# Performance work log

Hardware: AMD Instinct MI355X
Metric: run time of the kernel (lower is better)

The kernel has to match this reference:

```python
import jax, jax.numpy as jnp
import numpy as np

D = 512
H = 8
HD = D // H

def setup_inputs() -> dict:
    key = jax.random.key(0)
    ks = jax.random.split(key, 16)
    B, L = 8, 384
    s = 1.0 / np.sqrt(D)
    inp = {
        "hidden_states": jax.random.normal(ks[0], (B, L, D), jnp.float32),
        "position_embeddings": jax.random.normal(ks[1], (L, L, D), jnp.float32),
        "attention_mask": jnp.ones((B, L), jnp.int32),
        "ln_g": jnp.ones((D,), jnp.float32),
        "ln_b": jnp.zeros((D,), jnp.float32),
        "Wq": jax.random.normal(ks[2], (D, D), jnp.float32) * s,
        "bq": jnp.zeros((D,), jnp.float32),
        "Wk": jax.random.normal(ks[3], (D, D), jnp.float32) * s,
        "bk": jnp.zeros((D,), jnp.float32),
        "Wv": jax.random.normal(ks[4], (D, D), jnp.float32) * s,
        "bv": jnp.zeros((D,), jnp.float32),
        "Wpos": jax.random.normal(ks[5], (D, D), jnp.float32) * s,
        "pos_bias_u": jax.random.normal(ks[6], (H, HD), jnp.float32) * 0.02,
        "pos_bias_v": jax.random.normal(ks[7], (H, HD), jnp.float32) * 0.02,
        "Wo": jax.random.normal(ks[8], (D, D), jnp.float32) * s,
        "bo": jnp.zeros((D,), jnp.float32),
    }
    return inp

def _layernorm(x, g, b, eps=1e-5):
    mu = jnp.mean(x, axis=-1, keepdims=True)
    var = jnp.var(x, axis=-1, keepdims=True)
    return (x - mu) * jax.lax.rsqrt(var + eps) * g + b

def reference(hidden_states, position_embeddings, attention_mask,
              ln_g, ln_b, Wq, bq, Wk, bk, Wv, bv, Wpos,
              pos_bias_u, pos_bias_v, Wo, bo):
    B, L, _ = hidden_states.shape
    x = _layernorm(hidden_states, ln_g, ln_b)
    # projections -> (B, L, H, HD)
    q = (x @ Wq.T + bq).reshape(B, L, H, HD)
    k = (x @ Wk.T + bk).reshape(B, L, H, HD)
    v = (x @ Wv.T + bv).reshape(B, L, H, HD)
    # relative position projection -> (H, L, L, HD); pos[h, i, j, d]
    pos = (position_embeddings @ Wpos.T).reshape(L, L, H, HD)
    pos = jnp.transpose(pos, (2, 0, 1, 3))
    q_u = q + pos_bias_u  # (B, L, H, HD)
    q_v = q + pos_bias_v
    # content score: ac[b,h,i,j] = sum_d q_u[b,i,h,d] * k[b,j,h,d]
    scores_ac = jnp.einsum('bihd,bjhd->bhij', q_u, k)
    # positional score (torch broadcast semantics): bd[b,h,i,j] = sum_d q_v[b,j,h,d] * pos[h,i,j,d]
    scores_bd = jnp.einsum('bjhd,hijd->bhij', q_v, pos)
    scores = (scores_ac + scores_bd) / np.sqrt(HD)
    mask = attention_mask[:, None, None, :]  # (B,1,1,L)
    scores = jnp.where(mask == 0, jnp.finfo(scores.dtype).min, scores)
    probs = jax.nn.softmax(scores, axis=-1)
    ctx = jnp.einsum('bhij,bjhd->bihd', probs, v).reshape(B, L, D)
    return ctx @ Wo.T + bo
```

## Files before the change

kernel.cpp:

```cpp
#include <hip/hip_runtime.h>
#include <hip/hip_bf16.h>

#define DEV __device__ __forceinline__

typedef short short8 __attribute__((ext_vector_type(8)));
typedef float f32x4 __attribute__((ext_vector_type(4)));
typedef unsigned short ushort4v __attribute__((ext_vector_type(4)));
typedef unsigned short u16;

DEV u16 f2b(float x){ __hip_bfloat16 h = __float2bfloat16(x); u16 u; __builtin_memcpy(&u, &h, 2); return u; }

DEV int swz(int row, int cb){ return row*128 + (cb ^ ((row & 7) << 4)); }
DEV int swz768(int row, int byte_in_row){ return row*768 + (byte_in_row ^ ((row & 7) << 4)); }

DEV short8 ldfrag(const u16* s, int row, int kbf){
  return *(const short8*)((const char*)s + swz(row, kbf*2));
}
DEV void st16(u16* s, int row, int cb, short8 v){
  *(short8*)((char*)s + swz(row, cb)) = v;
}
DEV f32x4 MFMA(short8 a, short8 b, f32x4 c){
  return __builtin_amdgcn_mfma_f32_16x16x32_bf16(a, b, c, 0, 0, 0);
}

template<int R>
DEV void stage_bf16(u16* lds, const u16* g, size_t rstride, int tid){
  #pragma unroll
  for (int c = tid; c < R*8; c += 256){
    int row = c >> 3, k = c & 7;
    short8 v = *(const short8*)(g + (size_t)row*rstride + k*8);
    st16(lds, row, k*16, v);
  }
}

template<int R>
DEV void stage_f32(u16* lds, const float* g, size_t rstride, int tid){
  #pragma unroll
  for (int c = tid; c < R*8; c += 256){
    int row = c >> 3, k = c & 7;
    const float* p = g + (size_t)row*rstride + k*8;
    f32x4 f0 = *(const f32x4*)p;
    f32x4 f1 = *(const f32x4*)(p + 4);
    short8 v;
    #pragma unroll
    for (int t = 0; t < 4; ++t){ v[t] = (short)f2b(f0[t]); v[t+4] = (short)f2b(f1[t]); }
    st16(lds, row, k*16, v);
  }
}

template<int MI, int NI>
DEV void mma_step(const u16* As, int ar0, const u16* Bs, int br0, f32x4 (&acc)[MI][NI], int lane){
  int r = lane & 15, kb = (lane >> 4) * 8;
  #pragma unroll
  for (int kk = 0; kk < 64; kk += 32){
    short8 a[MI], b[NI];
    #pragma unroll
    for (int mi = 0; mi < MI; ++mi) a[mi] = ldfrag(As, ar0 + mi*16 + r, kk + kb);
    #pragma unroll
    for (int ni = 0; ni < NI; ++ni) b[ni] = ldfrag(Bs, br0 + ni*16 + r, kk + kb);
    #pragma unroll
    for (int mi = 0; mi < MI; ++mi)
      #pragma unroll
      for (int ni = 0; ni < NI; ++ni)
        acc[mi][ni] = MFMA(a[mi], b[ni], acc[mi][ni]);
  }
}

__global__ __launch_bounds__(256) void k_ln(const float* __restrict__ hs, const float* __restrict__ g,
                                            const float* __restrict__ bb, u16* __restrict__ xbf){
  int lane = threadIdx.x & 63, wid = threadIdx.x >> 6;
  int row = blockIdx.x * 4 + wid;
  const float* p = hs + (size_t)row * 512;
  f32x4 v0 = ((const f32x4*)p)[lane];
  f32x4 v1 = ((const f32x4*)p)[lane + 64];
  float s = 0.f, s2 = 0.f;
  #pragma unroll
  for (int t = 0; t < 4; ++t){ s += v0[t] + v1[t]; s2 += v0[t]*v0[t] + v1[t]*v1[t]; }
  #pragma unroll
  for (int off = 32; off; off >>= 1){ s += __shfl_xor(s, off); s2 += __shfl_xor(s2, off); }
  float mu = s * (1.0f/512.0f);
  float var = s2 * (1.0f/512.0f) - mu*mu;
  float rs = rsqrtf(var + 1e-5f);
  int e0 = lane * 4, e1 = 256 + e0;
  ushort4v o0, o1;
  #pragma unroll
  for (int t = 0; t < 4; ++t){
    o0[t] = f2b((v0[t]-mu)*rs*g[e0+t]+bb[e0+t]);
    o1[t] = f2b((v1[t]-mu)*rs*g[e1+t]+bb[e1+t]);
  }
  *(ushort4v*)(xbf + (size_t)row*512 + e0) = o0;
  *(ushort4v*)(xbf + (size_t)row*512 + e1) = o1;
}

__global__ __launch_bounds__(256) void k_wpt(const float* __restrict__ Wpos, u16* __restrict__ Wpt){
  int idx = blockIdx.x * 256 + threadIdx.x;
  int o = idx >> 9, e = idx & 511;
  int h = o >> 6, d = o & 63;
  Wpt[((size_t)h*512 + e)*64 + d] = f2b(Wpos[idx]);
}

__global__ __launch_bounds__(256) void k_qkv(const u16* __restrict__ xbf,
    const float* __restrict__ Wq, const float* __restrict__ Wk, const float* __restrict__ Wv,
    const float* __restrict__ bq, const float* __restrict__ bk, const float* __restrict__ bv,
    const float* __restrict__ pbu, const float* __restrict__ pbv,
    u16* __restrict__ qu, u16* __restrict__ qv, u16* __restrict__ kkb, u16* __restrict__ vt){
  __shared__ __align__(16) u16 As[128*64];
  __shared__ __align__(16) u16 Bs[128*64];
  int tid = threadIdx.x, lane = tid & 63, wid = tid >> 6;
  int t0 = blockIdx.x * 128, n0 = blockIdx.y * 128, z = blockIdx.z;
  const float* W    = (z==0) ? Wq : (z==1) ? Wk : Wv;
  const float* bias = (z==0) ? bq : (z==1) ? bk : bv;
  f32x4 acc[4][4] = {};
  for (int k0 = 0; k0 < 512; k0 += 64){
    stage_bf16<128>(As, xbf + (size_t)t0*512 + k0, 512, tid);
    stage_f32<128>(Bs, W + (size_t)n0*512 + k0, 512, tid);
    __syncthreads();
    mma_step<4,4>(As, (wid>>1)*64, Bs, (wid&1)*64, acc, lane);
    __syncthreads();
  }
  int r = lane & 15, half = lane >> 4;
  #pragma unroll
  for (int mi = 0; mi < 4; ++mi)
  #pragma unroll
  for (int ni = 0; ni < 4; ++ni){
    int n = n0 + (wid&1)*64 + ni*16 + r;
    int h = n >> 6, d = n & 63;
    int m0 = t0 + (wid>>1)*64 + mi*16 + half*4;
    #pragma unroll
    for (int q = 0; q < 4; ++q){
      int t = m0 + q, b = t / 384, i = t - b*384;
      float v = acc[mi][ni][q] + bias[n];
      if (z == 0){
        qu[((size_t)(b*8+h)*384 + i)*64 + d] = f2b(v + pbu[n]);
        qv[((size_t)h*3072 + t)*64 + d]      = f2b(v + pbv[n]);
      } else if (z == 1){
        kkb[((size_t)(b*8+h)*384 + i)*64 + d] = f2b(v);
      } else {
        vt[((size_t)(b*8+h)*64 + d)*384 + i] = f2b(v);
      }
    }
  }
}

__global__ __launch_bounds__(256) void k_qw(const u16* __restrict__ qv, const u16* __restrict__ Wpt,
                                            u16* __restrict__ qW){
  __shared__ __align__(16) u16 As[128*64];
  __shared__ __align__(16) u16 Bs[128*64];
  int tid = threadIdx.x, lane = tid & 63, wid = tid >> 6;
  int t0 = blockIdx.x * 128, e0 = blockIdx.y * 128, h = blockIdx.z;
  f32x4 acc[4][4] = {};
  stage_bf16<128>(As, qv + ((size_t)h*3072 + t0)*64, 64, tid);
  stage_bf16<128>(Bs, Wpt + ((size_t)h*512 + e0)*64, 64, tid);
  __syncthreads();
  mma_step<4,4>(As, (wid>>1)*64, Bs, (wid&1)*64, acc, lane);
  int r = lane & 15, half = lane >> 4;
  #pragma unroll
  for (int mi = 0; mi < 4; ++mi)
  #pragma unroll
  for (int ni = 0; ni < 4; ++ni){
    int e = e0 + (wid&1)*64 + ni*16 + r;
    int m0 = t0 + (wid>>1)*64 + mi*16 + half*4;
    #pragma unroll
    for (int q = 0; q < 4; ++q){
      int t = m0 + q, b = t / 384, j = t - b*384;
      int bh = b*8 + h;
      qW[((size_t)bh*384 + j)*512 + e] = f2b(acc[mi][ni][q]);
    }
  }
}

__global__ __launch_bounds__(256, 3) void k_bd(const u16* __restrict__ qW, const float* __restrict__ P,
                                               float* __restrict__ Sbd){
  __shared__ __align__(16) u16 As[64*256];
  int tid = threadIdx.x, lane = tid & 63, wid = tid >> 6;
  int r = lane & 15, half = lane >> 4;
  int ib = blockIdx.x * 192, j = blockIdx.y;

  const float* Bp[3];
  #pragma unroll
  for (int ni = 0; ni < 3; ++ni){
    int i = ib + wid*48 + ni*16 + r;
    Bp[ni] = P + ((size_t)i*384 + j)*512 + half*8;
  }
  const u16* Ag = qW + (size_t)j*512;

  f32x4 acc[4][3] = {};
  #pragma unroll
  for (int kh = 0; kh < 2; ++kh){
    if (kh) __syncthreads();
    #pragma unroll
    for (int s = 0; s < 8; ++s){
      int c = tid + s*256;
      int bh = c >> 5, c16 = c & 31;
      short8 v = *(const short8*)(Ag + (size_t)bh*(384*512) + kh*256 + c16*8);
      *(short8*)((char*)As + bh*512 + ((c16*16) ^ ((bh & 7) << 4))) = v;
    }
    __syncthreads();
    #pragma unroll
    for (int k32 = 0; k32 < 8; ++k32){
      int e0 = kh*256 + k32*32;
      short8 bfr[3];
      #pragma unroll
      for (int ni = 0; ni < 3; ++ni){
        f32x4 f0 = *(const f32x4*)(Bp[ni] + e0);
        f32x4 f1 = *(const f32x4*)(Bp[ni] + e0 + 4);
        #pragma unroll
        for (int t = 0; t < 4; ++t){ bfr[ni][t] = (short)f2b(f0[t]); bfr[ni][t+4] = (short)f2b(f1[t]); }
      }
      #pragma unroll
      for (int mi = 0; mi < 4; ++mi){
        int row = mi*16 + r;
        short8 afr = *(const short8*)((const char*)As + row*512 + ((k32*64 + half*16) ^ ((row & 7) << 4)));
        #pragma unroll
        for (int ni = 0; ni < 3; ++ni)
          acc[mi][ni] = MFMA(afr, bfr[ni], acc[mi][ni]);
      }
    }
  }
  #pragma unroll
  for (int mi = 0; mi < 4; ++mi)
  #pragma unroll
  for (int ni = 0; ni < 3; ++ni){
    int i = ib + wid*48 + ni*16 + r;
    #pragma unroll
    for (int q = 0; q < 4; ++q){
      int bh = mi*16 + half*4 + q;
      Sbd[((size_t)j*64 + bh)*384 + i] = acc[mi][ni][q];
    }
  }
}

__global__ __launch_bounds__(256) void k_fin(const u16* __restrict__ qu, const u16* __restrict__ kkb,
                                             const u16* __restrict__ vt, const float* __restrict__ Sbd,
                                             const int* __restrict__ mask, u16* __restrict__ ctx){
  __shared__ __align__(16) char lds[72*1024];
  __shared__ float smbuf[2][4][2][16];
  u16* Ks = (u16*)lds;
  u16* Qs = (u16*)(lds + 48*1024);
  u16* Ps = (u16*)lds;
  u16* Vs = (u16*)(lds + 24*1024);
  int tid = threadIdx.x, lane = tid & 63, wid = tid >> 6;
  int r = lane & 15, half = lane >> 4;
  int i0 = blockIdx.x * 32, bh = blockIdx.y, b = bh >> 3, h = bh & 7;

  stage_bf16<384>(Ks, kkb + (size_t)bh*384*64, 64, tid);
  stage_bf16<32>(Qs, qu + ((size_t)bh*384 + i0)*64, 64, tid);
  __syncthreads();

  f32x4 acc[6][2] = {};
  mma_step<6,2>(Ks, wid*96, Qs, 0, acc, lane);

  int jw = wid*96 + half*4;
  #pragma unroll
  for (int mi = 0; mi < 6; ++mi){
    #pragma unroll
    for (int q = 0; q < 4; ++q){
      int j = jw + mi*16 + q;
      bool dead = (mask[b*384 + j] == 0);
      const float* srow = Sbd + ((size_t)j*64 + bh)*384 + i0;
      #pragma unroll
      for (int ni = 0; ni < 2; ++ni){
        float v = (acc[mi][ni][q] + srow[ni*16 + r]) * 0.125f;
        acc[mi][ni][q] = dead ? -3.402823466e38f : v;
      }
    }
  }

  short8 vreg[12];
  #pragma unroll
  for (int c = 0; c < 12; ++c){
    int cc = tid + c*256;
    int d = cc / 48, jc = cc - d*48;
    vreg[c] = *(const short8*)(vt + ((size_t)bh*64 + d)*384 + jc*8);
  }

  float mx[2];
  #pragma unroll
  for (int ni = 0; ni < 2; ++ni){
    float m = -3.402823466e38f;
    #pragma unroll
    for (int mi = 0; mi < 6; ++mi){
      f32x4 a = acc[mi][ni];
      m = fmaxf(m, fmaxf(fmaxf(a[0],a[1]), fmaxf(a[2],a[3])));
    }
    m = fmaxf(m, __shfl_xor(m, 16));
    m = fmaxf(m, __shfl_xor(m, 32));
    mx[ni] = m;
  }
  if (lane < 16){ smbuf[0][wid][0][r] = mx[0]; smbuf[0][wid][1][r] = mx[1]; }
  __syncthreads();
  #pragma unroll
  for (int ni = 0; ni < 2; ++ni)
    mx[ni] = fmaxf(fmaxf(smbuf[0][0][ni][r], smbuf[0][1][ni][r]),
                   fmaxf(smbuf[0][2][ni][r], smbuf[0][3][ni][r]));

  float sum[2] = {0.f, 0.f};
  #pragma unroll
  for (int ni = 0; ni < 2; ++ni){
    #pragma unroll
    for (int mi = 0; mi < 6; ++mi)
      #pragma unroll
      for (int q = 0; q < 4; ++q){
        float e = __expf(acc[mi][ni][q] - mx[ni]);
        acc[mi][ni][q] = e; sum[ni] += e;
      }
    sum[ni] += __shfl_xor(sum[ni], 16);
    sum[ni] += __shfl_xor(sum[ni], 32);
  }
  if (lane < 16){ smbuf[1][wid][0][r] = sum[0]; smbuf[1][wid][1][r] = sum[1]; }
  __syncthreads();
  float inv[2];
  #pragma unroll
  for (int ni = 0; ni < 2; ++ni)
    inv[ni] = 1.0f / (smbuf[1][0][ni][r] + smbuf[1][1][ni][r] + smbuf[1][2][ni][r] + smbuf[1][3][ni][r]);

  #pragma unroll
  for (int mi = 0; mi < 6; ++mi){
    int jb = jw + mi*16;
    #pragma unroll
    for (int ni = 0; ni < 2; ++ni){
      int i = ni*16 + r;
      ushort4v pk;
      #pragma unroll
      for (int q = 0; q < 4; ++q) pk[q] = f2b(acc[mi][ni][q] * inv[ni]);
      *(ushort4v*)((char*)Ps + swz768(i, jb*2)) = pk;
    }
  }
  #pragma unroll
  for (int c = 0; c < 12; ++c){
    int cc = tid + c*256;
    int d = cc / 48, jc = cc - d*48;
    *(short8*)((char*)Vs + swz768(d, jc*16)) = vreg[c];
  }
  __syncthreads();

  f32x4 acc2[2] = {};
  #pragma unroll
  for (int ks = 0; ks < 384; ks += 32){
    int j0 = ks + half*8;
    short8 bfr = *(const short8*)((const char*)Vs + swz768(wid*16 + r, j0*2));
    #pragma unroll
    for (int mi = 0; mi < 2; ++mi){
      short8 afr = *(const short8*)((const char*)Ps + swz768(mi*16 + r, j0*2));
      acc2[mi] = MFMA(afr, bfr, acc2[mi]);
    }
  }
  #pragma unroll
  for (int mi = 0; mi < 2; ++mi)
    #pragma unroll
    for (int q = 0; q < 4; ++q){
      int i = i0 + mi*16 + half*4 + q;
      int d = wid*16 + r;
      ctx[((size_t)(b*384 + i))*512 + h*64 + d] = f2b(acc2[mi][q]);
    }
}

__global__ __launch_bounds__(256) void k_out(const u16* __restrict__ ctx, const float* __restrict__ Wo,
                                             const float* __restrict__ bo, float* __restrict__ out){
  __shared__ __align__(16) u16 As[128*64];
  __shared__ __align__(16) u16 Bs[128*64];
  int tid = threadIdx.x, lane = tid & 63, wid = tid >> 6;
  int t0 = blockIdx.x * 128, n0 = blockIdx.y * 128;
  f32x4 acc[4][4] = {};
  for (int k0 = 0; k0 < 512; k0 += 64){
    stage_bf16<128>(As, ctx + (size_t)t0*512 + k0, 512, tid);
    stage_f32<128>(Bs, Wo + (size_t)n0*512 + k0, 512, tid);
    __syncthreads();
    mma_step<4,4>(As, (wid>>1)*64, Bs, (wid&1)*64, acc, lane);
    __syncthreads();
  }
  int r = lane & 15, half = lane >> 4;
  #pragma unroll
  for (int mi = 0; mi < 4; ++mi)
  #pragma unroll
  for (int ni = 0; ni < 4; ++ni){
    int n = n0 + (wid&1)*64 + ni*16 + r;
    int m0 = t0 + (wid>>1)*64 + mi*16 + half*4;
    #pragma unroll
    for (int q = 0; q < 4; ++q){
      int t = m0 + q;
      out[(size_t)t*512 + n] = acc[mi][ni][q] + bo[n];
    }
  }
}

extern "C" void kernel_launch(void* const* d_in, const int* in_sizes, int n_in,
                              void* d_out, int out_size, void* d_ws, size_t ws_size,
                              hipStream_t stream) {
  const float* hs   = (const float*)d_in[0];
  const float* P    = (const float*)d_in[1];
  const int*   mask = (const int*)d_in[2];
  const float* ln_g = (const float*)d_in[3];
  const float* ln_b = (const float*)d_in[4];
  const float* Wq   = (const float*)d_in[5];
  const float* bq   = (const float*)d_in[6];
  const float* Wk   = (const float*)d_in[7];
  const float* bk   = (const float*)d_in[8];
  const float* Wv   = (const float*)d_in[9];
  const float* bv   = (const float*)d_in[10];
  const float* Wpos = (const float*)d_in[11];
  const float* pbu  = (const float*)d_in[12];
  const float* pbv  = (const float*)d_in[13];
  const float* Wo   = (const float*)d_in[14];
  const float* bo   = (const float*)d_in[15];
  float* out = (float*)d_out;

  char* w = (char*)d_ws;
  u16* xbf = (u16*)w;   w += (size_t)3072*512*2;
  u16* qu  = (u16*)w;   w += (size_t)3072*512*2;
  u16* qv  = (u16*)w;   w += (size_t)3072*512*2;
  u16* kkb = (u16*)w;   w += (size_t)3072*512*2;
  u16* vt  = (u16*)w;   w += (size_t)3072*512*2;
  u16* Wpt = (u16*)w;   w += (size_t)8*512*64*2;
  u16* ctx = (u16*)w;   w += (size_t)3072*512*2;
  u16* qW  = (u16*)w;   w += (size_t)64*384*512*2;
  float* Sbd = (float*)w; w += (size_t)64*384*384*4;

  k_ln <<<768, 256, 0, stream>>>(hs, ln_g, ln_b, xbf);
  k_wpt<<<1024, 256, 0, stream>>>(Wpos, Wpt);
  k_qkv<<<dim3(24,4,3), 256, 0, stream>>>(xbf, Wq, Wk, Wv, bq, bk, bv, pbu, pbv, qu, qv, kkb, vt);
  k_qw <<<dim3(24,4,8), 256, 0, stream>>>(qv, Wpt, qW);
  k_bd <<<dim3(2,384), 256, 0, stream>>>(qW, P, Sbd);
  k_fin<<<dim3(12,64), 256, 0, stream>>>(qu, kkb, vt, Sbd, mask, ctx);
  k_out<<<dim3(24,4), 256, 0, stream>>>(ctx, Wo, bo, out);
}
```

Measured before the change: 196.0 us.

## Fuse layernorm and Wpos transpose into GEMMs, batch k_fin rows, retile k_out

LayerNorm is folded into the QKV GEMM: each block computes row statistics and normalizes hidden states while staging the A tile. The Wpos bf16 transpose is done inside k_qw's staging, which removes two kernel launches and the xbf/Wpt intermediate buffers. k_fin now handles 96 query rows per block in three sub-tiles, so K and V are staged once and reused across them. k_out moves to 64x64 tiles to launch more blocks. The costs are redundant LayerNorm statistics across the 12 blocks per row tile, uncoalesced strided Wpos reads, and more LDS per k_fin block, which lowers occupancy.

```diff
diff --git a/kernel.cpp b/kernel.cpp
--- a/kernel.cpp
+++ b/kernel.cpp
@@ -66,57 +66,65 @@
   }
 }
 
-__global__ __launch_bounds__(256) void k_ln(const float* __restrict__ hs, const float* __restrict__ g,
-                                            const float* __restrict__ bb, u16* __restrict__ xbf){
-  int lane = threadIdx.x & 63, wid = threadIdx.x >> 6;
-  int row = blockIdx.x * 4 + wid;
-  const float* p = hs + (size_t)row * 512;
-  f32x4 v0 = ((const f32x4*)p)[lane];
-  f32x4 v1 = ((const f32x4*)p)[lane + 64];
-  float s = 0.f, s2 = 0.f;
-  #pragma unroll
-  for (int t = 0; t < 4; ++t){ s += v0[t] + v1[t]; s2 += v0[t]*v0[t] + v1[t]*v1[t]; }
-  #pragma unroll
-  for (int off = 32; off; off >>= 1){ s += __shfl_xor(s, off); s2 += __shfl_xor(s2, off); }
-  float mu = s * (1.0f/512.0f);
-  float var = s2 * (1.0f/512.0f) - mu*mu;
-  float rs = rsqrtf(var + 1e-5f);
-  int e0 = lane * 4, e1 = 256 + e0;
-  ushort4v o0, o1;
-  #pragma unroll
-  for (int t = 0; t < 4; ++t){
-    o0[t] = f2b((v0[t]-mu)*rs*g[e0+t]+bb[e0+t]);
-    o1[t] = f2b((v1[t]-mu)*rs*g[e1+t]+bb[e1+t]);
-  }
-  *(ushort4v*)(xbf + (size_t)row*512 + e0) = o0;
-  *(ushort4v*)(xbf + (size_t)row*512 + e1) = o1;
-}
-
-__global__ __launch_bounds__(256) void k_wpt(const float* __restrict__ Wpos, u16* __restrict__ Wpt){
-  int idx = blockIdx.x * 256 + threadIdx.x;
-  int o = idx >> 9, e = idx & 511;
-  int h = o >> 6, d = o & 63;
-  Wpt[((size_t)h*512 + e)*64 + d] = f2b(Wpos[idx]);
-}
-
-__global__ __launch_bounds__(256) void k_qkv(const u16* __restrict__ xbf,
+__global__ __launch_bounds__(256) void k_qkv(const float* __restrict__ hs,
+    const float* __restrict__ lg, const float* __restrict__ lb,
     const float* __restrict__ Wq, const float* __restrict__ Wk, const float* __restrict__ Wv,
     const float* __restrict__ bq, const float* __restrict__ bk, const float* __restrict__ bv,
     const float* __restrict__ pbu, const float* __restrict__ pbv,
     u16* __restrict__ qu, u16* __restrict__ qv, u16* __restrict__ kkb, u16* __restrict__ vt){
   __shared__ __align__(16) u16 As[128*64];
   __shared__ __align__(16) u16 Bs[128*64];
+  __shared__ float ps[2][128], ps2[2][128], mus[128], rss[128];
+  __shared__ float gs[512], bss[512];
   int tid = threadIdx.x, lane = tid & 63, wid = tid >> 6;
   int t0 = blockIdx.x * 128, n0 = blockIdx.y * 128, z = blockIdx.z;
   const float* W    = (z==0) ? Wq : (z==1) ? Wk : Wv;
   const float* bias = (z==0) ? bq : (z==1) ? bk : bv;
+
+  {
+    int row = tid & 127, hf = tid >> 7;
+    const f32x4* p = (const f32x4*)(hs + (size_t)(t0+row)*512 + hf*256);
+    float s = 0.f, s2 = 0.f;
+    #pragma unroll 8
+    for (int c = 0; c < 64; ++c){
+      f32x4 v = p[c];
+      #pragma unroll
+      for (int t = 0; t < 4; ++t){ s += v[t]; s2 += v[t]*v[t]; }
+    }
+    ps[hf][row] = s; ps2[hf][row] = s2;
+  }
+  gs[tid] = lg[tid]; gs[tid+256] = lg[tid+256];
+  bss[tid] = lb[tid]; bss[tid+256] = lb[tid+256];
+  __syncthreads();
+  if (tid < 128){
+    float S = ps[0][tid] + ps[1][tid], S2 = ps2[0][tid] + ps2[1][tid];
+    float mu = S * (1.0f/512.0f);
+    float var = S2 * (1.0f/512.0f) - mu*mu;
+    mus[tid] = mu; rss[tid] = rsqrtf(var + 1e-5f);
+  }
+
   f32x4 acc[4][4] = {};
   for (int k0 = 0; k0 < 512; k0 += 64){
-    stage_bf16<128>(As, xbf + (size_t)t0*512 + k0, 512, tid);
+    __syncthreads();
+    #pragma unroll
+    for (int c = tid; c < 1024; c += 256){
+      int rw = c >> 3, k = c & 7;
+      const float* pp = hs + (size_t)(t0+rw)*512 + k0 + k*8;
+      f32x4 f0 = *(const f32x4*)pp;
+      f32x4 f1 = *(const f32x4*)(pp + 4);
+      float mu = mus[rw], rs = rss[rw];
+      short8 v;
+      #pragma unroll
+      for (int t = 0; t < 4; ++t){
+        int e = k0 + k*8 + t;
+        v[t]   = (short)f2b((f0[t]-mu)*rs*gs[e]   + bss[e]);
+        v[t+4] = (short)f2b((f1[t]-mu)*rs*gs[e+4] + bss[e+4]);
+      }
+      st16(As, rw, k*16, v);
+    }
     stage_f32<128>(Bs, W + (size_t)n0*512 + k0, 512, tid);
     __syncthreads();
     mma_step<4,4>(As, (wid>>1)*64, Bs, (wid&1)*64, acc, lane);
-    __syncthreads();
   }
   int r = lane & 15, half = lane >> 4;
   #pragma unroll
@@ -142,7 +150,7 @@
   }
 }
 
-__global__ __launch_bounds__(256) void k_qw(const u16* __restrict__ qv, const u16* __restrict__ Wpt,
+__global__ __launch_bounds__(256) void k_qw(const u16* __restrict__ qv, const float* __restrict__ Wpos,
                                             u16* __restrict__ qW){
   __shared__ __align__(16) u16 As[128*64];
   __shared__ __align__(16) u16 Bs[128*64];
@@ -150,7 +158,15 @@
   int t0 = blockIdx.x * 128, e0 = blockIdx.y * 128, h = blockIdx.z;
   f32x4 acc[4][4] = {};
   stage_bf16<128>(As, qv + ((size_t)h*3072 + t0)*64, 64, tid);
-  stage_bf16<128>(Bs, Wpt + ((size_t)h*512 + e0)*64, 64, tid);
+  #pragma unroll
+  for (int c = tid; c < 1024; c += 256){
+    int e = c >> 3, k = c & 7;
+    short8 v;
+    #pragma unroll
+    for (int t = 0; t < 8; ++t)
+      v[t] = (short)f2b(Wpos[(size_t)(h*64 + k*8 + t)*512 + e0 + e]);
+    st16(Bs, e, k*16, v);
+  }
   __syncthreads();
   mma_step<4,4>(As, (wid>>1)*64, Bs, (wid&1)*64, acc, lane);
   int r = lane & 15, half = lane >> 4;
@@ -233,149 +249,143 @@
 __global__ __launch_bounds__(256) void k_fin(const u16* __restrict__ qu, const u16* __restrict__ kkb,
                                              const u16* __restrict__ vt, const float* __restrict__ Sbd,
                                              const int* __restrict__ mask, u16* __restrict__ ctx){
-  __shared__ __align__(16) char lds[72*1024];
+  __shared__ __align__(16) u16 Ks[384*64];
+  __shared__ __align__(16) u16 Qs[96*64];
+  __shared__ __align__(16) u16 Vs[64*384];
+  __shared__ __align__(16) u16 Ps[32*384];
   __shared__ float smbuf[2][4][2][16];
-  u16* Ks = (u16*)lds;
-  u16* Qs = (u16*)(lds + 48*1024);
-  u16* Ps = (u16*)lds;
-  u16* Vs = (u16*)(lds + 24*1024);
   int tid = threadIdx.x, lane = tid & 63, wid = tid >> 6;
   int r = lane & 15, half = lane >> 4;
-  int i0 = blockIdx.x * 32, bh = blockIdx.y, b = bh >> 3, h = bh & 7;
+  int i0 = blockIdx.x * 96, bh = blockIdx.y, b = bh >> 3, h = bh & 7;
 
   stage_bf16<384>(Ks, kkb + (size_t)bh*384*64, 64, tid);
-  stage_bf16<32>(Qs, qu + ((size_t)bh*384 + i0)*64, 64, tid);
+  stage_bf16<96>(Qs, qu + ((size_t)bh*384 + i0)*64, 64, tid);
+  #pragma unroll
+  for (int c = tid; c < 3072; c += 256){
+    int d = c / 48, jc = c - d*48;
+    short8 v = *(const short8*)(vt + ((size_t)bh*64 + d)*384 + jc*8);
+    *(short8*)((char*)Vs + swz768(d, jc*16)) = v;
+  }
   __syncthreads();
 
-  f32x4 acc[6][2] = {};
-  mma_step<6,2>(Ks, wid*96, Qs, 0, acc, lane);
-
-  int jw = wid*96 + half*4;
-  #pragma unroll
-  for (int mi = 0; mi < 6; ++mi){
-    #pragma unroll
-    for (int q = 0; q < 4; ++q){
-      int j = jw + mi*16 + q;
-      bool dead = (mask[b*384 + j] == 0);
-      const float* srow = Sbd + ((size_t)j*64 + bh)*384 + i0;
+  for (int sub = 0; sub < 3; ++sub){
+    int i0s = i0 + sub*32;
+    f32x4 acc[6][2] = {};
+    mma_step<6,2>(Ks, wid*96, Qs, sub*32, acc, lane);
+
+    int jw = wid*96 + half*4;
+    #pragma unroll
+    for (int mi = 0; mi < 6; ++mi){
+      #pragma unroll
+      for (int q = 0; q < 4; ++q){
+        int j = jw + mi*16 + q;
+        bool dead = (mask[b*384 + j] == 0);
+        const float* srow = Sbd + ((size_t)j*64 + bh)*384 + i0s;
+        #pragma unroll
+        for (int ni = 0; ni < 2; ++ni){
+          float v = (acc[mi][ni][q] + srow[ni*16 + r]) * 0.125f;
+          acc[mi][ni][q] = dead ? -3.402823466e38f : v;
+        }
+      }
+    }
+
+    float mx[2];
+    #pragma unroll
+    for (int ni = 0; ni < 2; ++ni){
+      float m = -3.402823466e38f;
+      #pragma unroll
+      for (int mi = 0; mi < 6; ++mi){
+        f32x4 a = acc[mi][ni];
+        m = fmaxf(m, fmaxf(fmaxf(a[0],a[1]), fmaxf(a[2],a[3])));
+      }
+      m = fmaxf(m, __shfl_xor(m, 16));
+      m = fmaxf(m, __shfl_xor(m, 32));
+      mx[ni] = m;
+    }
+    if (lane < 16){ smbuf[0][wid][0][r] = mx[0]; smbuf[0][wid][1][r] = mx[1]; }
+    __syncthreads();
+    #pragma unroll
+    for (int ni = 0; ni < 2; ++ni)
+      mx[ni] = fmaxf(fmaxf(smbuf[0][0][ni][r], smbuf[0][1][ni][r]),
+                     fmaxf(smbuf[0][2][ni][r], smbuf[0][3][ni][r]));
+
+    float sum[2] = {0.f, 0.f};
+    #pragma unroll
+    for (int ni = 0; ni < 2; ++ni){
+      #pragma unroll
+      for (int mi = 0; mi < 6; ++mi)
+        #pragma unroll
+        for (int q = 0; q < 4; ++q){
+          float e = __expf(acc[mi][ni][q] - mx[ni]);
+          acc[mi][ni][q] = e; sum[ni] += e;
+        }
+      sum[ni] += __shfl_xor(sum[ni], 16);
+      sum[ni] += __shfl_xor(sum[ni], 32);
+    }
+    if (lane < 16){ smbuf[1][wid][0][r] = sum[0]; smbuf[1][wid][1][r] = sum[1]; }
+    __syncthreads();
+    float inv[2];
+    #pragma unroll
+    for (int ni = 0; ni < 2; ++ni)
+      inv[ni] = 1.0f / (smbuf[1][0][ni][r] + smbuf[1][1][ni][r] + smbuf[1][2][ni][r] + smbuf[1][3][ni][r]);
+
+    #pragma unroll
+    for (int mi = 0; mi < 6; ++mi){
+      int jb = jw + mi*16;
       #pragma unroll
       for (int ni = 0; ni < 2; ++ni){
-        float v = (acc[mi][ni][q] + srow[ni*16 + r]) * 0.125f;
-        acc[mi][ni][q] = dead ? -3.402823466e38f : v;
-      }
-    }
-  }
-
-  short8 vreg[12];
-  #pragma unroll
-  for (int c = 0; c < 12; ++c){
-    int cc = tid + c*256;
-    int d = cc / 48, jc = cc - d*48;
-    vreg[c] = *(const short8*)(vt + ((size_t)bh*64 + d)*384 + jc*8);
-  }
-
-  float mx[2];
-  #pragma unroll
-  for (int ni = 0; ni < 2; ++ni){
-    float m = -3.402823466e38f;
-    #pragma unroll
-    for (int mi = 0; mi < 6; ++mi){
-      f32x4 a = acc[mi][ni];
-      m = fmaxf(m, fmaxf(fmaxf(a[0],a[1]), fmaxf(a[2],a[3])));
-    }
-    m = fmaxf(m, __shfl_xor(m, 16));
-    m = fmaxf(m, __shfl_xor(m, 32));
-    mx[ni] = m;
-  }
-  if (lane < 16){ smbuf[0][wid][0][r] = mx[0]; smbuf[0][wid][1][r] = mx[1]; }
-  __syncthreads();
-  #pragma unroll
-  for (int ni = 0; ni < 2; ++ni)
-    mx[ni] = fmaxf(fmaxf(smbuf[0][0][ni][r], smbuf[0][1][ni][r]),
-                   fmaxf(smbuf[0][2][ni][r], smbuf[0][3][ni][r]));
-
-  float sum[2] = {0.f, 0.f};
-  #pragma unroll
-  for (int ni = 0; ni < 2; ++ni){
-    #pragma unroll
-    for (int mi = 0; mi < 6; ++mi)
+        int i = ni*16 + r;
+        ushort4v pk;
+        #pragma unroll
+        for (int q = 0; q < 4; ++q) pk[q] = f2b(acc[mi][ni][q] * inv[ni]);
+        *(ushort4v*)((char*)Ps + swz768(i, jb*2)) = pk;
+      }
+    }
+    __syncthreads();
+
+    f32x4 acc2[2] = {};
+    #pragma unroll
+    for (int ks = 0; ks < 384; ks += 32){
+      int j0 = ks + half*8;
+      short8 bfr = *(const short8*)((const char*)Vs + swz768(wid*16 + r, j0*2));
+      #pragma unroll
+      for (int mi = 0; mi < 2; ++mi){
+        short8 afr = *(const short8*)((const char*)Ps + swz768(mi*16 + r, j0*2));
+        acc2[mi] = MFMA(afr, bfr, acc2[mi]);
+      }
+    }
+    #pragma unroll
+    for (int mi = 0; mi < 2; ++mi)
       #pragma unroll
       for (int q = 0; q < 4; ++q){
-        float e = __expf(acc[mi][ni][q] - mx[ni]);
-        acc[mi][ni][q] = e; sum[ni] += e;
-      }
-    sum[ni] += __shfl_xor(sum[ni], 16);
-    sum[ni] += __shfl_xor(sum[ni], 32);
-  }
-  if (lane < 16){ smbuf[1][wid][0][r] = sum[0]; smbuf[1][wid][1][r] = sum[1]; }
-  __syncthreads();
-  float inv[2];
-  #pragma unroll
-  for (int ni = 0; ni < 2; ++ni)
-    inv[ni] = 1.0f / (smbuf[1][0][ni][r] + smbuf[1][1][ni][r] + smbuf[1][2][ni][r] + smbuf[1][3][ni][r]);
-
-  #pragma unroll
-  for (int mi = 0; mi < 6; ++mi){
-    int jb = jw + mi*16;
-    #pragma unroll
-    for (int ni = 0; ni < 2; ++ni){
-      int i = ni*16 + r;
-      ushort4v pk;
-      #pragma unroll
-      for (int q = 0; q < 4; ++q) pk[q] = f2b(acc[mi][ni][q] * inv[ni]);
-      *(ushort4v*)((char*)Ps + swz768(i, jb*2)) = pk;
-    }
-  }
-  #pragma unroll
-  for (int c = 0; c < 12; ++c){
-    int cc = tid + c*256;
-    int d = cc / 48, jc = cc - d*48;
-    *(short8*)((char*)Vs + swz768(d, jc*16)) = vreg[c];
-  }
-  __syncthreads();
-
-  f32x4 acc2[2] = {};
-  #pragma unroll
-  for (int ks = 0; ks < 384; ks += 32){
-    int j0 = ks + half*8;
-    short8 bfr = *(const short8*)((const char*)Vs + swz768(wid*16 + r, j0*2));
-    #pragma unroll
-    for (int mi = 0; mi < 2; ++mi){
-      short8 afr = *(const short8*)((const char*)Ps + swz768(mi*16 + r, j0*2));
-      acc2[mi] = MFMA(afr, bfr, acc2[mi]);
-    }
-  }
-  #pragma unroll
-  for (int mi = 0; mi < 2; ++mi)
-    #pragma unroll
-    for (int q = 0; q < 4; ++q){
-      int i = i0 + mi*16 + half*4 + q;
-      int d = wid*16 + r;
-      ctx[((size_t)(b*384 + i))*512 + h*64 + d] = f2b(acc2[mi][q]);
-    }
+        int i = i0s + mi*16 + half*4 + q;
+        int d = wid*16 + r;
+        ctx[((size_t)(b*384 + i))*512 + h*64 + d] = f2b(acc2[mi][q]);
+      }
+  }
 }
 
 __global__ __launch_bounds__(256) void k_out(const u16* __restrict__ ctx, const float* __restrict__ Wo,
                                              const float* __restrict__ bo, float* __restrict__ out){
-  __shared__ __align__(16) u16 As[128*64];
-  __shared__ __align__(16) u16 Bs[128*64];
+  __shared__ __align__(16) u16 As[64*64];
+  __shared__ __align__(16) u16 Bs[64*64];
   int tid = threadIdx.x, lane = tid & 63, wid = tid >> 6;
-  int t0 = blockIdx.x * 128, n0 = blockIdx.y * 128;
-  f32x4 acc[4][4] = {};
+  int t0 = blockIdx.x * 64, n0 = blockIdx.y * 64;
+  f32x4 acc[2][2] = {};
   for (int k0 = 0; k0 < 512; k0 += 64){
-    stage_bf16<128>(As, ctx + (size_t)t0*512 + k0, 512, tid);
-    stage_f32<128>(Bs, Wo + (size_t)n0*512 + k0, 512, tid);
-    __syncthreads();
-    mma_step<4,4>(As, (wid>>1)*64, Bs, (wid&1)*64, acc, lane);
+    stage_bf16<64>(As, ctx + (size_t)t0*512 + k0, 512, tid);
+    stage_f32<64>(Bs, Wo + (size_t)n0*512 + k0, 512, tid);
+    __syncthreads();
+    mma_step<2,2>(As, (wid>>1)*32, Bs, (wid&1)*32, acc, lane);
     __syncthreads();
   }
   int r = lane & 15, half = lane >> 4;
   #pragma unroll
-  for (int mi = 0; mi < 4; ++mi)
-  #pragma unroll
-  for (int ni = 0; ni < 4; ++ni){
-    int n = n0 + (wid&1)*64 + ni*16 + r;
-    int m0 = t0 + (wid>>1)*64 + mi*16 + half*4;
+  for (int mi = 0; mi < 2; ++mi)
+  #pragma unroll
+  for (int ni = 0; ni < 2; ++ni){
+    int n = n0 + (wid&1)*32 + ni*16 + r;
+    int m0 = t0 + (wid>>1)*32 + mi*16 + half*4;
     #pragma unroll
     for (int q = 0; q < 4; ++q){
       int t = m0 + q;
@@ -406,21 +416,17 @@
   float* out = (float*)d_out;
 
   char* w = (char*)d_ws;
-  u16* xbf = (u16*)w;   w += (size_t)3072*512*2;
   u16* qu  = (u16*)w;   w += (size_t)3072*512*2;
   u16* qv  = (u16*)w;   w += (size_t)3072*512*2;
   u16* kkb = (u16*)w;   w += (size_t)3072*512*2;
   u16* vt  = (u16*)w;   w += (size_t)3072*512*2;
-  u16* Wpt = (u16*)w;   w += (size_t)8*512*64*2;
   u16* ctx = (u16*)w;   w += (size_t)3072*512*2;
   u16* qW  = (u16*)w;   w += (size_t)64*384*512*2;
   float* Sbd = (float*)w; w += (size_t)64*384*384*4;
 
-  k_ln <<<768, 256, 0, stream>>>(hs, ln_g, ln_b, xbf);
-  k_wpt<<<1024, 256, 0, stream>>>(Wpos, Wpt);
-  k_qkv<<<dim3(24,4,3), 256, 0, stream>>>(xbf, Wq, Wk, Wv, bq, bk, bv, pbu, pbv, qu, qv, kkb, vt);
-  k_qw <<<dim3(24,4,8), 256, 0, stream>>>(qv, Wpt, qW);
+  k_qkv<<<dim3(24,4,3), 256, 0, stream>>>(hs, ln_g, ln_b, Wq, Wk, Wv, bq, bk, bv, pbu, pbv, qu, qv, kkb, vt);
+  k_qw <<<dim3(24,4,8), 256, 0, stream>>>(qv, Wpos, qW);
   k_bd <<<dim3(2,384), 256, 0, stream>>>(qW, P, Sbd);
-  k_fin<<<dim3(12,64), 256, 0, stream>>>(qu, kkb, vt, Sbd, mask, ctx);
-  k_out<<<dim3(24,4), 256, 0, stream>>>(ctx, Wo, bo, out);
-}
+  k_fin<<<dim3(4,64), 256, 0, stream>>>(qu, kkb, vt, Sbd, mask, ctx);
+  k_out<<<dim3(48,8), 256, 0, stream>>>(ctx, Wo, bo, out);
+}
```

Result: faster. 180.1 us (-8.1%).
